# Kernel tuning notes

Hardware: AMD Instinct MI355X
Metric: run time of the kernel (lower is better)

Reference implementation:

```python
import jax, jax.numpy as jnp
import numpy as np

EPSILON = 0.1      # max offset magnitude relative to anchor norm (init kwarg)
NORM_EPS = 1e-12   # F.normalize denom clamp
DIV_EPS = 1e-8     # offset-norm division eps


def setup_inputs() -> dict:
    key = jax.random.key(0)
    k1, k2 = jax.random.split(key)
    embeddings = jax.random.normal(k1, (4, 2048, 2048), dtype=jnp.float32)
    vocab_embeddings = jax.random.normal(k2, (32000, 2048), dtype=jnp.float32)
    return {"embeddings": embeddings, "vocab_embeddings": vocab_embeddings}


def reference(embeddings, vocab_embeddings):
    B, S, D = embeddings.shape
    x = embeddings.reshape(-1, D)                                   # [BS, D]
    xn = x / jnp.maximum(jnp.linalg.norm(x, axis=-1, keepdims=True), NORM_EPS)
    vn = vocab_embeddings / jnp.maximum(
        jnp.linalg.norm(vocab_embeddings, axis=-1, keepdims=True), NORM_EPS)
    sim = xn @ vn.T                                                 # [BS, V]
    anchor_ids = jnp.argmax(sim, axis=-1)                           # [BS]
    anchor = vocab_embeddings[anchor_ids]                           # [BS, D]
    offset = x - anchor
    offset_norm = jnp.linalg.norm(offset, axis=-1, keepdims=True)
    anchor_norm = jnp.linalg.norm(anchor, axis=-1, keepdims=True)
    scale = jnp.minimum(EPSILON * anchor_norm / (offset_norm + DIV_EPS), 1.0)
    result = anchor + offset * scale
    return result.reshape(B, S, D), anchor_ids.reshape(B, S)
```

## Files before the change

kernel.cpp:

```cpp
#include <hip/hip_runtime.h>
#include <hip/hip_bf16.h>

#define DIM 2048
#define BM 128
#define BN 256
#define BK 64
#define KSTEPS (DIM / BK)
#define A_TILE_BYTES (BM * BK)
#define B_TILE_BYTES (BN * BK)
#define NLEV 8

typedef _Float16 f16x8 __attribute__((ext_vector_type(8)));
typedef float f32x4 __attribute__((ext_vector_type(4)));
typedef int i32x4 __attribute__((ext_vector_type(4)));
typedef unsigned long long u64;

#define INV_SX 27.6f
#define INV_SVN 1150.0f

typedef const unsigned int __attribute__((address_space(1))) gu32;
typedef unsigned int __attribute__((address_space(3))) lu32;

__device__ __forceinline__ void gl_lds16(const void* g, void* l) {
    __builtin_amdgcn_global_load_lds((gu32*)g, (lu32*)l, 16, 0, 0);
}

__device__ __forceinline__ u64 pack_key(float v, unsigned int col) {
    unsigned int b = __float_as_uint(v);
    b ^= (unsigned int)(((int)b >> 31)) | 0x80000000u;
    return ((u64)b << 32) | (u64)(~col);
}
__device__ __forceinline__ u64 pack_key_i(int dot, unsigned int col) {
    unsigned int b = (unsigned int)dot ^ 0x80000000u;
    return ((u64)b << 32) | (u64)(~col);
}
__device__ __forceinline__ u64 umax64(u64 a, u64 b) { return a > b ? a : b; }
__device__ __forceinline__ u64 umin64(u64 a, u64 b) { return a < b ? a : b; }

__device__ __forceinline__ void cascadeN(u64* Rrow, int stride, u64 k) {
    if (k <= Rrow[(NLEV - 1) * stride]) return;
#pragma unroll
    for (int l = 0; l < NLEV; ++l) {
        u64 old = atomicMax(&Rrow[l * stride], k);
        k = umin64(k, old);
        if (!k) return;
    }
}
__device__ __forceinline__ void cascade3(u64* r1, u64* r2, u64* r3, u64 k) {
    u64 old = atomicMax(r1, k);
    k = umin64(k, old);
    if (k) {
        old = atomicMax(r2, k);
        k = umin64(k, old);
        if (k) atomicMax(r3, k);
    }
}

__device__ __forceinline__ int toff(int row, int kg) {
    const int line = row >> 1;
    const int s8 = ((row & 1) << 2) | kg;
    return line * 128 + ((s8 ^ (line & 7)) << 4);
}

__device__ __forceinline__ int swz(int row, int slot) {
    return row * 32 + (slot ^ ((row >> 1) & 3)) * 8;
}

__global__ void vocab_invnorm_kernel(const float* __restrict__ Vg,
                                     float* __restrict__ invnorm) {
    const int v = blockIdx.x;
    const int t = threadIdx.x;
    const float* row = Vg + (size_t)v * DIM;
    float4 f0 = *reinterpret_cast<const float4*>(row + t * 8);
    float4 f1 = *reinterpret_cast<const float4*>(row + t * 8 + 4);
    float s = f0.x*f0.x + f0.y*f0.y + f0.z*f0.z + f0.w*f0.w
            + f1.x*f1.x + f1.y*f1.y + f1.z*f1.z + f1.w*f1.w;
#pragma unroll
    for (int off = 32; off > 0; off >>= 1) s += __shfl_down(s, off);
    __shared__ float ls[4];
    const int lane = t & 63, w = t >> 6;
    if (lane == 0) ls[w] = s;
    __syncthreads();
    if (t == 0) {
        float tot = ls[0] + ls[1] + ls[2] + ls[3];
        invnorm[v] = 1.0f / fmaxf(sqrtf(tot), 1e-12f);
    }
}

__device__ __forceinline__ int q16pack(const float* xv, float s, int base, int* out4) {
#pragma unroll
    for (int g = 0; g < 4; ++g) {
        int p = 0;
#pragma unroll
        for (int e = 0; e < 4; ++e) {
            int q = __float2int_rn(xv[base + g * 4 + e] * s);
            q = q > 127 ? 127 : (q < -127 ? -127 : q);
            p |= (q & 255) << (e * 8);
        }
        out4[g] = p;
    }
    return 0;
}

__global__ void convert_x_q(const float* __restrict__ X, signed char* __restrict__ Xq) {
    const int tile = blockIdx.x;
    const int mblk = tile >> 5, ks = tile & 31;
    const float* src = X + (size_t)(mblk * BM) * DIM + ks * BK;
    signed char* dst = Xq + (size_t)tile * A_TILE_BYTES;
    const int t = threadIdx.x;
#pragma unroll
    for (int u = 0; u < 2; ++u) {
        const int c = t + u * 256;
        const int line = c >> 3;
        const int s8 = (c & 7) ^ (line & 7);
        const int row = (line << 1) | (s8 >> 2);
        const int cs = s8 & 3;
        const float* s = src + (size_t)row * DIM + cs * 16;
        float xv[16];
        *(float4*)(&xv[0])  = *(const float4*)(s);
        *(float4*)(&xv[4])  = *(const float4*)(s + 4);
        *(float4*)(&xv[8])  = *(const float4*)(s + 8);
        *(float4*)(&xv[12]) = *(const float4*)(s + 12);
        int q4[4];
        q16pack(xv, INV_SX, 0, q4);
        *(int4*)(dst + c * 16) = make_int4(q4[0], q4[1], q4[2], q4[3]);
    }
}

__global__ void convert_v_q(const float* __restrict__ Vg,
                            const float* __restrict__ invnorm,
                            signed char* __restrict__ Vq) {
    const int tile = blockIdx.x;
    const int nblk = tile >> 5, ks = tile & 31;
    const float* src = Vg + (size_t)(nblk * BN) * DIM + ks * BK;
    signed char* dst = Vq + (size_t)tile * B_TILE_BYTES;
    const int t = threadIdx.x;
#pragma unroll
    for (int u = 0; u < 4; ++u) {
        const int c = t + u * 256;
        const int line = c >> 3;
        const int s8 = (c & 7) ^ (line & 7);
        const int row = (line << 1) | (s8 >> 2);
        const int cs = s8 & 3;
        const float sc = invnorm[nblk * BN + row] * INV_SVN;
        const float* s = src + (size_t)row * DIM + cs * 16;
        float xv[16];
        *(float4*)(&xv[0])  = *(const float4*)(s);
        *(float4*)(&xv[4])  = *(const float4*)(s + 4);
        *(float4*)(&xv[8])  = *(const float4*)(s + 8);
        *(float4*)(&xv[12]) = *(const float4*)(s + 12);
        int q4[4];
        q16pack(xv, sc, 0, q4);
        *(int4*)(dst + c * 16) = make_int4(q4[0], q4[1], q4[2], q4[3]);
    }
}

__global__ __launch_bounds__(512, 4) void sim_i8_dual(
        const signed char* __restrict__ Xq, const signed char* __restrict__ Vq,
        u64* __restrict__ R, int M) {
    __shared__ alignas(16) signed char ldsA[2][A_TILE_BYTES];
    __shared__ alignas(16) signed char ldsB[2][B_TILE_BYTES];

    const int tid = threadIdx.x;
    const int flat = blockIdx.x;
    const int idx  = (flat & 7) * 1000 + (flat >> 3);
    const int mblk = idx & 63;
    const int nblk = idx >> 6;

    const int lane = tid & 63;
    const int w  = tid >> 6;
    const int wm = w >> 2, wn = w & 3;
    const int lr = lane & 15;
    const int kg = lane >> 4;

    const signed char* Atiles = Xq + (size_t)mblk * KSTEPS * A_TILE_BYTES;
    const signed char* Btiles = Vq + (size_t)nblk * KSTEPS * B_TILE_BYTES;

    i32x4 acc[4][4] = {};

    int offA[4], offB[4];
#pragma unroll
    for (int i = 0; i < 4; ++i) offA[i] = toff(wm * 64 + i * 16 + lr, kg);
#pragma unroll
    for (int j = 0; j < 4; ++j) offB[j] = toff(wn * 64 + j * 16 + lr, kg);

    const int cA  = tid * 16;
    const int cB1 = tid * 16;
    const int cB2 = (tid + 512) * 16;

    gl_lds16(Atiles + cA,  &ldsA[0][cA]);
    gl_lds16(Btiles + cB1, &ldsB[0][cB1]);
    gl_lds16(Btiles + cB2, &ldsB[0][cB2]);
    __syncthreads();

    int cur = 0;
    for (int ks = 0; ks < KSTEPS; ++ks) {
        if (ks + 1 < KSTEPS) {
            const signed char* an = Atiles + (size_t)(ks + 1) * A_TILE_BYTES;
            const signed char* bn = Btiles + (size_t)(ks + 1) * B_TILE_BYTES;
            gl_lds16(an + cA,  &ldsA[cur ^ 1][cA]);
            gl_lds16(bn + cB1, &ldsB[cur ^ 1][cB1]);
            gl_lds16(bn + cB2, &ldsB[cur ^ 1][cB2]);
        }
        i32x4 bhf[4];
#pragma unroll
        for (int j = 0; j < 4; ++j) bhf[j] = *(const i32x4*)(&ldsB[cur][offB[j]]);
#pragma unroll
        for (int i = 0; i < 4; ++i) {
            i32x4 ahf = *(const i32x4*)(&ldsA[cur][offA[i]]);
#pragma unroll
            for (int j = 0; j < 4; ++j)
                acc[i][j] = __builtin_amdgcn_mfma_i32_16x16x64_i8(ahf, bhf[j], acc[i][j], 0, 0, 0);
        }
        __syncthreads();
        cur ^= 1;
    }

    const int m0 = mblk * BM, n0 = nblk * BN;
#pragma unroll
    for (int i = 0; i < 4; ++i) {
#pragma unroll
        for (int r = 0; r < 4; ++r) {
            u64 k[4];
#pragma unroll
            for (int j = 0; j < 4; ++j)
                k[j] = pack_key_i(acc[i][j][r],
                                  (unsigned int)(n0 + wn * 64 + j * 16 + lr));
            u64 m01 = umax64(k[0], k[1]), n01 = umin64(k[0], k[1]);
            u64 m23 = umax64(k[2], k[3]), n23 = umin64(k[2], k[3]);
            u64 a1k = umax64(m01, m23);
            u64 a2k = umax64(umin64(m01, m23), umax64(n01, n23));
#pragma unroll
            for (int mask = 1; mask < 16; mask <<= 1) {
                u64 o1 = __shfl_xor(a1k, mask);
                u64 o2 = __shfl_xor(a2k, mask);
                u64 t1 = umax64(a1k, o1);
                a2k = umax64(umin64(a1k, o1), umax64(a2k, o2));
                a1k = t1;
            }
            if (lr == 0) {
                const int row = m0 + wm * 64 + i * 16 + kg * 4 + r;
                cascadeN(&R[row], M, a1k);
                cascadeN(&R[row], M, a2k);
            }
        }
    }
}

__global__ __launch_bounds__(256) void sim_coarse_fallback(
        const float* __restrict__ X, const float* __restrict__ Vg,
        const float* __restrict__ invnorm,
        u64* __restrict__ R1, u64* __restrict__ R2, u64* __restrict__ R3) {
    __shared__ alignas(16) _Float16 Ah[128 * 32];
    __shared__ alignas(16) _Float16 Bh[128 * 32];
    const int tid = threadIdx.x;
    const int flat = blockIdx.x;
    const int idx  = (flat & 7) * 2000 + (flat >> 3);
    const int panel = idx / 3200;
    const int w_    = idx - panel * 3200;
    const int mblk  = w_ & 63;
    const int nblk  = panel * 50 + (w_ >> 6);
    const int m0 = mblk * 128, n0 = nblk * 128;
    const int lane = tid & 63;
    const int w  = tid >> 6;
    const int wm = w >> 1, wn = w & 1;
    const int lr = lane & 15;
    const int kg = lane >> 4;
    const int sr  = tid >> 2;
    const int skc = tid & 3;
    const float* Aptr0 = X  + (size_t)(m0 + sr)      * DIM + skc * 8;
    const float* Aptr1 = X  + (size_t)(m0 + 64 + sr) * DIM + skc * 8;
    const float* Bptr0 = Vg + (size_t)(n0 + sr)      * DIM + skc * 8;
    const float* Bptr1 = Vg + (size_t)(n0 + 64 + sr) * DIM + skc * 8;
    float4 ra[4], rb[4];
    ra[0] = *(const float4*)(Aptr0);     ra[1] = *(const float4*)(Aptr0 + 4);
    ra[2] = *(const float4*)(Aptr1);     ra[3] = *(const float4*)(Aptr1 + 4);
    rb[0] = *(const float4*)(Bptr0);     rb[1] = *(const float4*)(Bptr0 + 4);
    rb[2] = *(const float4*)(Bptr1);     rb[3] = *(const float4*)(Bptr1 + 4);
    f32x4 acc[4][4] = {};
    const int wA0 = swz(sr, skc), wA1 = swz(sr + 64, skc);
    for (int ks = 0; ks < 64; ++ks) {
        {
            f16x8 h; float xv[8];
            *(float4*)(&xv[0]) = ra[0]; *(float4*)(&xv[4]) = ra[1];
#pragma unroll
            for (int e = 0; e < 8; ++e) h[e] = (_Float16)xv[e];
            *(f16x8*)(&Ah[wA0]) = h;
            *(float4*)(&xv[0]) = ra[2]; *(float4*)(&xv[4]) = ra[3];
#pragma unroll
            for (int e = 0; e < 8; ++e) h[e] = (_Float16)xv[e];
            *(f16x8*)(&Ah[wA1]) = h;
            *(float4*)(&xv[0]) = rb[0]; *(float4*)(&xv[4]) = rb[1];
#pragma unroll
            for (int e = 0; e < 8; ++e) h[e] = (_Float16)xv[e];
            *(f16x8*)(&Bh[wA0]) = h;
            *(float4*)(&xv[0]) = rb[2]; *(float4*)(&xv[4]) = rb[3];
#pragma unroll
            for (int e = 0; e < 8; ++e) h[e] = (_Float16)xv[e];
            *(f16x8*)(&Bh[wA1]) = h;
        }
        __syncthreads();
        if (ks + 1 < 64) {
            const int ko = (ks + 1) * 32;
            ra[0] = *(const float4*)(Aptr0 + ko); ra[1] = *(const float4*)(Aptr0 + ko + 4);
            ra[2] = *(const float4*)(Aptr1 + ko); ra[3] = *(const float4*)(Aptr1 + ko + 4);
            rb[0] = *(const float4*)(Bptr0 + ko); rb[1] = *(const float4*)(Bptr0 + ko + 4);
            rb[2] = *(const float4*)(Bptr1 + ko); rb[3] = *(const float4*)(Bptr1 + ko + 4);
        }
        f16x8 bhf[4];
#pragma unroll
        for (int j = 0; j < 4; ++j)
            bhf[j] = *(const f16x8*)(&Bh[swz(wn * 64 + j * 16 + lr, kg)]);
#pragma unroll
        for (int i = 0; i < 4; ++i) {
            f16x8 ahf = *(const f16x8*)(&Ah[swz(wm * 64 + i * 16 + lr, kg)]);
#pragma unroll
            for (int j = 0; j < 4; ++j)
                acc[i][j] = __builtin_amdgcn_mfma_f32_16x16x32_f16(ahf, bhf[j], acc[i][j], 0, 0, 0);
        }
        __syncthreads();
    }
    float inv[4];
#pragma unroll
    for (int j = 0; j < 4; ++j) inv[j] = invnorm[n0 + wn * 64 + j * 16 + lr];
#pragma unroll
    for (int i = 0; i < 4; ++i) {
#pragma unroll
        for (int r = 0; r < 4; ++r) {
            u64 k[4];
#pragma unroll
            for (int j = 0; j < 4; ++j)
                k[j] = pack_key(acc[i][j][r] * inv[j],
                                (unsigned int)(n0 + wn * 64 + j * 16 + lr));
            u64 m01 = umax64(k[0], k[1]), n01 = umin64(k[0], k[1]);
            u64 m23 = umax64(k[2], k[3]), n23 = umin64(k[2], k[3]);
            u64 a1 = umax64(m01, m23);
            u64 a2 = umax64(umin64(m01, m23), umax64(n01, n23));
#pragma unroll
            for (int mask = 1; mask < 16; mask <<= 1) {
                u64 b1 = __shfl_xor(a1, mask);
                u64 b2 = __shfl_xor(a2, mask);
                u64 t1 = umax64(a1, b1);
                a2 = umax64(umin64(a1, b1), umax64(a2, b2));
                a1 = t1;
            }
            if (lr == 0) {
                const int row = m0 + wm * 64 + i * 16 + kg * 4 + r;
                cascade3(&R1[row], &R2[row], &R3[row], a1);
                cascade3(&R1[row], &R2[row], &R3[row], a2);
            }
        }
    }
}

__device__ __forceinline__ float block_sum(float v, float* sbuf, int t) {
#pragma unroll
    for (int off = 32; off > 0; off >>= 1) v += __shfl_down(v, off);
    const int lane = t & 63, w = t >> 6;
    __syncthreads();
    if (lane == 0) sbuf[w] = v;
    __syncthreads();
    return sbuf[0] + sbuf[1] + sbuf[2] + sbuf[3];
}

__global__ void rescue_finalize_kernel(const float* __restrict__ X,
                                       const float* __restrict__ Vg,
                                       const u64* __restrict__ R, int M, int NV,
                                       float* __restrict__ outx,
                                       float* __restrict__ outid) {
    const int row = blockIdx.x;
    const int t = threadIdx.x;
    __shared__ float sbuf[4];

    int cand[NLEV];
#pragma unroll
    for (int c = 0; c < NLEV; ++c) {
        unsigned int id = ~(unsigned int)(R[c * M + row] & 0xFFFFFFFFull);
        cand[c] = (id < (unsigned int)NV) ? (int)id : 0;
    }

    const float* x = X + (size_t)row * DIM;
    float4 x0 = *reinterpret_cast<const float4*>(x + t * 8);
    float4 x1 = *reinterpret_cast<const float4*>(x + t * 8 + 4);
    float xxp = x0.x*x0.x + x0.y*x0.y + x0.z*x0.z + x0.w*x0.w
              + x1.x*x1.x + x1.y*x1.y + x1.z*x1.z + x1.w*x1.w;
    const float xx = block_sum(xxp, sbuf, t);
    const float xn = fmaxf(sqrtf(xx), 1e-12f);

    u64 bestkey = 0ull;
    int bestid = cand[0];
    float bestsa = 0.f;
#pragma unroll
    for (int c = 0; c < NLEV; ++c) {
        const float* v = Vg + (size_t)cand[c] * DIM;
        float4 v0 = *reinterpret_cast<const float4*>(v + t * 8);
        float4 v1 = *reinterpret_cast<const float4*>(v + t * 8 + 4);
        float dp = x0.x*v0.x + x0.y*v0.y + x0.z*v0.z + x0.w*v0.w
                 + x1.x*v1.x + x1.y*v1.y + x1.z*v1.z + x1.w*v1.w;
        float vp = v0.x*v0.x + v0.y*v0.y + v0.z*v0.z + v0.w*v0.w
                 + v1.x*v1.x + v1.y*v1.y + v1.z*v1.z + v1.w*v1.w;
        const float dot = block_sum(dp, sbuf, t);
        const float vv  = block_sum(vp, sbuf, t);
        const float s = dot / (xn * fmaxf(sqrtf(vv), 1e-12f));
        u64 key = pack_key(s, (unsigned int)cand[c]);
        if (key > bestkey) { bestkey = key; bestid = cand[c]; bestsa = vv; }
    }

    const float* a = Vg + (size_t)bestid * DIM;
    float4 a0 = *reinterpret_cast<const float4*>(a + t * 8);
    float4 a1 = *reinterpret_cast<const float4*>(a + t * 8 + 4);
    float4 d0 = make_float4(x0.x-a0.x, x0.y-a0.y, x0.z-a0.z, x0.w-a0.w);
    float4 d1 = make_float4(x1.x-a1.x, x1.y-a1.y, x1.z-a1.z, x1.w-a1.w);
    float sop = d0.x*d0.x + d0.y*d0.y + d0.z*d0.z + d0.w*d0.w
              + d1.x*d1.x + d1.y*d1.y + d1.z*d1.z + d1.w*d1.w;
    const float so = block_sum(sop, sbuf, t);
    const float scale = fminf(0.1f * sqrtf(bestsa) / (sqrtf(so) + 1e-8f), 1.0f);

    float4 o0 = make_float4(a0.x + d0.x*scale, a0.y + d0.y*scale,
                            a0.z + d0.z*scale, a0.w + d0.w*scale);
    float4 o1 = make_float4(a1.x + d1.x*scale, a1.y + d1.y*scale,
                            a1.z + d1.z*scale, a1.w + d1.w*scale);
    float* o = outx + (size_t)row * DIM + t * 8;
    *reinterpret_cast<float4*>(o)     = o0;
    *reinterpret_cast<float4*>(o + 4) = o1;
    if (t == 0) outid[row] = (float)bestid;
}

extern "C" void kernel_launch(void* const* d_in, const int* in_sizes, int n_in,
                              void* d_out, int out_size, void* d_ws, size_t ws_size,
                              hipStream_t stream) {
    const float* X  = (const float*)d_in[0];
    const float* Vg = (const float*)d_in[1];
    const int M  = in_sizes[0] / DIM;
    const int NV = in_sizes[1] / DIM;

    char* ws = (char*)d_ws;
    u64* R = (u64*)ws;
    size_t off = (size_t)NLEV * M * sizeof(u64);
    float* invnorm = (float*)(ws + off);
    off += ((size_t)NV * sizeof(float) + 255) & ~255ull;
    signed char* Xq = (signed char*)(ws + off);
    off += (size_t)M * DIM;
    signed char* Vq = (signed char*)(ws + off);
    off += (size_t)NV * DIM;
    const bool fast = (ws_size >= off);

    float* outx  = (float*)d_out;
    float* outid = outx + (size_t)M * DIM;

    hipMemsetAsync(R, 0, (size_t)NLEV * M * sizeof(u64), stream);
    vocab_invnorm_kernel<<<NV, 256, 0, stream>>>(Vg, invnorm);

    if (fast) {
        convert_x_q<<<(M / BM) * KSTEPS, 256, 0, stream>>>(X, Xq);
        convert_v_q<<<(NV / BN) * KSTEPS, 256, 0, stream>>>(Vg, invnorm, Vq);
        dim3 grid((NV / BN) * (M / BM));
        sim_i8_dual<<<grid, 512, 0, stream>>>(Xq, Vq, R, M);
    } else {
        dim3 gridf((NV / 128) * (M / 128));
        sim_coarse_fallback<<<gridf, 256, 0, stream>>>(X, Vg, invnorm,
                                                       R, R + M, R + 2 * M);
    }

    rescue_finalize_kernel<<<M, 256, 0, stream>>>(X, Vg, R, M, NV, outx, outid);
}
```

Before: 1.314 ms.

## Load B operand fragments directly from global into registers, skipping LDS

The int8 similarity GEMM now loads each wave's B (vocab) fragments straight from global memory into registers, prefetching the next k-step's fragments while the current MFMAs run. The B tiles no longer go through LDS, which halves-plus the shared memory footprint and removes the LDS read traffic for B. The cost is that B is no longer shared across the two M-waves, so each B fragment is fetched from global or L2 twice. Global-load latency is also exposed if one step of prefetch is not enough.

```diff
diff --git a/kernel.cpp b/kernel.cpp
--- a/kernel.cpp
+++ b/kernel.cpp
@@ -87,19 +87,18 @@
     }
 }
 
-__device__ __forceinline__ int q16pack(const float* xv, float s, int base, int* out4) {
+__device__ __forceinline__ void q16pack(const float* xv, float s, int* out4) {
 #pragma unroll
     for (int g = 0; g < 4; ++g) {
         int p = 0;
 #pragma unroll
         for (int e = 0; e < 4; ++e) {
-            int q = __float2int_rn(xv[base + g * 4 + e] * s);
+            int q = __float2int_rn(xv[g * 4 + e] * s);
             q = q > 127 ? 127 : (q < -127 ? -127 : q);
             p |= (q & 255) << (e * 8);
         }
         out4[g] = p;
     }
-    return 0;
 }
 
 __global__ void convert_x_q(const float* __restrict__ X, signed char* __restrict__ Xq) {
@@ -122,7 +121,7 @@
         *(float4*)(&xv[8])  = *(const float4*)(s + 8);
         *(float4*)(&xv[12]) = *(const float4*)(s + 12);
         int q4[4];
-        q16pack(xv, INV_SX, 0, q4);
+        q16pack(xv, INV_SX, q4);
         *(int4*)(dst + c * 16) = make_int4(q4[0], q4[1], q4[2], q4[3]);
     }
 }
@@ -150,16 +149,15 @@
         *(float4*)(&xv[8])  = *(const float4*)(s + 8);
         *(float4*)(&xv[12]) = *(const float4*)(s + 12);
         int q4[4];
-        q16pack(xv, sc, 0, q4);
+        q16pack(xv, sc, q4);
         *(int4*)(dst + c * 16) = make_int4(q4[0], q4[1], q4[2], q4[3]);
     }
 }
 
-__global__ __launch_bounds__(512, 4) void sim_i8_dual(
+__global__ __launch_bounds__(512, 4) void sim_i8_breg(
         const signed char* __restrict__ Xq, const signed char* __restrict__ Vq,
         u64* __restrict__ R, int M) {
     __shared__ alignas(16) signed char ldsA[2][A_TILE_BYTES];
-    __shared__ alignas(16) signed char ldsB[2][B_TILE_BYTES];
 
     const int tid = threadIdx.x;
     const int flat = blockIdx.x;
@@ -184,35 +182,37 @@
 #pragma unroll
     for (int j = 0; j < 4; ++j) offB[j] = toff(wn * 64 + j * 16 + lr, kg);
 
-    const int cA  = tid * 16;
-    const int cB1 = tid * 16;
-    const int cB2 = (tid + 512) * 16;
-
-    gl_lds16(Atiles + cA,  &ldsA[0][cA]);
-    gl_lds16(Btiles + cB1, &ldsB[0][cB1]);
-    gl_lds16(Btiles + cB2, &ldsB[0][cB2]);
+    const int cA = tid * 16;
+
+    gl_lds16(Atiles + cA, &ldsA[0][cA]);
+    i32x4 b0 = *(const i32x4*)(Btiles + offB[0]);
+    i32x4 b1 = *(const i32x4*)(Btiles + offB[1]);
+    i32x4 b2 = *(const i32x4*)(Btiles + offB[2]);
+    i32x4 b3 = *(const i32x4*)(Btiles + offB[3]);
     __syncthreads();
 
     int cur = 0;
     for (int ks = 0; ks < KSTEPS; ++ks) {
+        const int nk = (ks + 1 < KSTEPS) ? (ks + 1) : ks;
+        const signed char* bn = Btiles + (size_t)nk * B_TILE_BYTES;
+        i32x4 nb0 = *(const i32x4*)(bn + offB[0]);
+        i32x4 nb1 = *(const i32x4*)(bn + offB[1]);
+        i32x4 nb2 = *(const i32x4*)(bn + offB[2]);
+        i32x4 nb3 = *(const i32x4*)(bn + offB[3]);
         if (ks + 1 < KSTEPS) {
             const signed char* an = Atiles + (size_t)(ks + 1) * A_TILE_BYTES;
-            const signed char* bn = Btiles + (size_t)(ks + 1) * B_TILE_BYTES;
-            gl_lds16(an + cA,  &ldsA[cur ^ 1][cA]);
-            gl_lds16(bn + cB1, &ldsB[cur ^ 1][cB1]);
-            gl_lds16(bn + cB2, &ldsB[cur ^ 1][cB2]);
-        }
-        i32x4 bhf[4];
-#pragma unroll
-        for (int j = 0; j < 4; ++j) bhf[j] = *(const i32x4*)(&ldsB[cur][offB[j]]);
+            gl_lds16(an + cA, &ldsA[cur ^ 1][cA]);
+        }
 #pragma unroll
         for (int i = 0; i < 4; ++i) {
             i32x4 ahf = *(const i32x4*)(&ldsA[cur][offA[i]]);
-#pragma unroll
-            for (int j = 0; j < 4; ++j)
-                acc[i][j] = __builtin_amdgcn_mfma_i32_16x16x64_i8(ahf, bhf[j], acc[i][j], 0, 0, 0);
+            acc[i][0] = __builtin_amdgcn_mfma_i32_16x16x64_i8(ahf, b0, acc[i][0], 0, 0, 0);
+            acc[i][1] = __builtin_amdgcn_mfma_i32_16x16x64_i8(ahf, b1, acc[i][1], 0, 0, 0);
+            acc[i][2] = __builtin_amdgcn_mfma_i32_16x16x64_i8(ahf, b2, acc[i][2], 0, 0, 0);
+            acc[i][3] = __builtin_amdgcn_mfma_i32_16x16x64_i8(ahf, b3, acc[i][3], 0, 0, 0);
         }
         __syncthreads();
+        b0 = nb0; b1 = nb1; b2 = nb2; b3 = nb3;
         cur ^= 1;
     }
 
@@ -455,7 +455,7 @@
         convert_x_q<<<(M / BM) * KSTEPS, 256, 0, stream>>>(X, Xq);
         convert_v_q<<<(NV / BN) * KSTEPS, 256, 0, stream>>>(Vg, invnorm, Vq);
         dim3 grid((NV / BN) * (M / BM));
-        sim_i8_dual<<<grid, 512, 0, stream>>>(Xq, Vq, R, M);
+        sim_i8_breg<<<grid, 512, 0, stream>>>(Xq, Vq, R, M);
     } else {
         dim3 gridf((NV / 128) * (M / 128));
         sim_coarse_fallback<<<gridf, 256, 0, stream>>>(X, Vg, invnorm,
```

After: 1.298 ms. About the same (-1.2%).
